# Kernel tuning notes

Hardware: AMD Instinct MI355X
Metric: run time of the kernel (lower is better)

The kernel has to match this reference:

```python
import jax, jax.numpy as jnp
import numpy as np

A_DIM = 6
VBR = jnp.array([300.0, 750.0, 1200.0, 1850.0, 2850.0, 4300.0])
MAX_BR = 4300.0
BUF = 30000.0  # buffer_size fixed to 30000 each forward
N_STEPS = 6    # unrolled iterations in the source (cooked_bw[0]..cooked_bw[5])


def _conv_feat(x, w, b):
    # 1-channel valid Conv1d(kernel=4) + ReLU, flattened channel-major like torch .view
    L = x.shape[0]
    idx = jnp.arange(L - 3)[:, None] + jnp.arange(4)[None, :]
    win = x[idx]                                   # (L-3, 4)
    out = jax.nn.relu(win @ w[:, 0, :].T + b)      # (L-3, 128)
    return out.T.reshape(-1)                       # (128*(L-3),)


def setup_inputs() -> dict:
    key = jax.random.key(0)
    ks = jax.random.split(key, 12)
    s = 0.1
    return {
        "inp": jax.random.uniform(ks[0], (8, 8), jnp.float32) + 0.1,
        "conv_w": jax.random.normal(ks[1], (128, 1, 4), jnp.float32) * s,
        "conv_b": jax.random.normal(ks[2], (128,), jnp.float32) * s,
        "w0": jax.random.normal(ks[3], (128, 1), jnp.float32) * s,
        "b0": jax.random.normal(ks[4], (128,), jnp.float32) * s,
        "w1": jax.random.normal(ks[5], (128, 1), jnp.float32) * s,
        "b1": jax.random.normal(ks[6], (128,), jnp.float32) * s,
        "w2": jax.random.normal(ks[7], (128, 1), jnp.float32) * s,
        "b2": jax.random.normal(ks[8], (128,), jnp.float32) * s,
        "w3": jax.random.normal(ks[9], (128, 2048), jnp.float32) * 0.02,
        "b3": jax.random.normal(ks[10], (128,), jnp.float32) * s,
        "w4": jax.random.normal(ks[11], (6, 128), jnp.float32) * s,
        "b4": jnp.zeros((6,), jnp.float32),
    }


def reference(inp, conv_w, conv_b, w0, b0, w1, b1, w2, b2, w3, b3, w4, b4):
    state = inp[:6, :]          # (6, 8)
    bw = inp[6, :]              # cooked bandwidth trace
    vs = inp[7, 0]              # base video chunk size
    vcs = vs * jnp.array([1.0, 2.0, 4.0, 8.0, 16.0, 32.0])  # video_chunk_sizes

    def net(st):
        s0 = jax.nn.relu(st[0, -1] * w0[:, 0] + b0)
        s1 = jax.nn.relu(st[1, -1] * w1[:, 0] + b1)
        s2 = _conv_feat(st[2, :], conv_w, conv_b)          # 640
        s3 = _conv_feat(st[3, :], conv_w, conv_b)          # 640
        s4 = _conv_feat(st[4, :A_DIM], conv_w, conv_b)     # 384
        s5 = st[4, -1] * w2[:, 0] + b2                     # no relu (matches source)
        feat = jnp.concatenate([s0, s1, s2, s3, s4, s5])   # (2048,)
        h = jax.nn.relu(w3 @ feat + b3)
        return w4 @ h + b4                                 # (6,)

    for i in range(N_STEPS):
        logits = net(state)
        a = jnp.argmax(logits)
        state = jnp.roll(state, -1, axis=1)
        delay = vcs[a] / bw[i] - BUF
        state = state.at[0, -1].set(VBR[a] / MAX_BR)
        state = state.at[1, -1].set(BUF / 1000.0 / 10.0)
        state = state.at[2, -1].set(vcs[a] / delay / 1000.0)
        state = state.at[3, -1].set(delay / 1000.0 / 10.0)
        state = state.at[4, :A_DIM].set(vcs / 1e6)
        state = state.at[5, -1].set((7.0 - i) / 8.0)

    return net(state)
```

## Files before the change

### kernel.cpp

```cpp
#include <hip/hip_runtime.h>

#define NBLK 32
#define TPB  256
#define FSTRIDE 32
#define PSTRIDE 64

__device__ __forceinline__ float relu_(float x) { return fmaxf(x, 0.f); }


__launch_bounds__(TPB, 1)
__global__ void actor_kernel(
    const float* __restrict__ inp,
    const float* __restrict__ conv_w, const float* __restrict__ conv_b,
    const float* __restrict__ w0, const float* __restrict__ b0,
    const float* __restrict__ w1, const float* __restrict__ b1,
    const float* __restrict__ w2, const float* __restrict__ b2,
    const float* __restrict__ w3, const float* __restrict__ b3,
    const float* __restrict__ w4, const float* __restrict__ b4,
    float* __restrict__ out, int* __restrict__ flags,
    float* __restrict__ partials)
{
    const int tid = threadIdx.x;
    const int b   = blockIdx.x;

    __shared__ __align__(16) float lw3[4 * 2048];
    __shared__ __align__(16) float lfeat[2048];
    __shared__ __align__(16) float lc2[512], lc3[512];
    __shared__ float lbase2[128], lbase3[128], ls5[128];
    __shared__ float ls0[6 * 128];
    __shared__ float ltmp[512];
    __shared__ __align__(16) float lcw[512];
    __shared__ float lcb[128];
    __shared__ float lw0v[128], lb0v[128], lw1v[128], lb1v[128];
    __shared__ float lw2v[128], lb2v[128], lb3v[128];
    __shared__ float lw4[768], lb4v[8];
    __shared__ float st2[8], st3[8], st4[8];
    __shared__ float sx[8];
    __shared__ float lbw[8];
    __shared__ float h_lds[4], hv_lds[4 * 8];
    __shared__ float red[48];
    __shared__ float s_red[192];
    __shared__ int   sact[2];

    {
        const float4* g4 = (const float4*)(w3 + b * 4 * 2048);
        float4* l4 = (float4*)lw3;
        for (int idx = tid; idx < 2048; idx += TPB) l4[idx] = g4[idx];
    }
    for (int idx = tid; idx < 512; idx += TPB) lcw[idx] = conv_w[idx];
    if (tid < 128) {
        lcb[tid]  = conv_b[tid];
        lw0v[tid] = w0[tid]; lb0v[tid] = b0[tid];
        lw1v[tid] = w1[tid]; lb1v[tid] = b1[tid];
        lw2v[tid] = w2[tid]; lb2v[tid] = b2[tid];
        lb3v[tid] = b3[tid];
    }
    for (int idx = tid; idx < 768; idx += TPB) lw4[idx] = w4[idx];
    if (tid < 6) lb4v[tid] = b4[tid];
    if (tid < 8) {
        st2[tid] = inp[16 + tid];
        st3[tid] = inp[24 + tid];
        st4[tid] = inp[32 + tid];
        lbw[tid] = inp[48 + tid];
    }
    if (tid == 0) {
        sx[0] = inp[7];   sx[1] = inp[15];
        sx[2] = inp[39];  sx[3] = inp[32];
        sx[4] = inp[56];
    }
    __syncthreads();

    if (tid < 128) {
        const float vb[6] = {300.f, 750.f, 1200.f, 1850.f, 2850.f, 4300.f};
        #pragma unroll
        for (int v = 0; v < 6; ++v)
            ls0[v * 128 + tid] = relu_(vb[v] * (1.f / 4300.f) * lw0v[tid] + lb0v[tid]);
        ltmp[tid] = relu_(3.0f * lw1v[tid] + lb1v[tid]);
    }
    for (int m = tid; m < 384; m += TPB) {
        int c = m / 3, w = m - c * 3;
        float a = lcb[c];
        #pragma unroll
        for (int k = 0; k < 4; ++k)
            a += sx[4] * (float)(1 << (w + k)) * 1e-6f * lcw[c * 4 + k];
        ltmp[128 + m] = relu_(a);
    }
    __syncthreads();

    const int wv = tid >> 6, lane = tid & 63;
    const float* wr = lw3 + wv * 2048;
    const float bias3 = lb3v[b * 4 + wv];

    float hs0p[6], hs14p;
    #pragma unroll
    for (int v = 0; v < 6; ++v)
        hs0p[v] = wr[lane] * ls0[v * 128 + lane] + wr[64 + lane] * ls0[v * 128 + 64 + lane];
    hs14p = wr[128 + lane] * ltmp[lane] + wr[192 + lane] * ltmp[64 + lane];
    #pragma unroll
    for (int k = 0; k < 6; ++k) {
        int m = lane + 64 * k;
        hs14p += wr[1536 + m] * ltmp[128 + m];
    }

    const float VBRc[6] = {300.f, 750.f, 1200.f, 1850.f, 2850.f, 4300.f};

    float fcom_f = 0.f;
    float lb2s[2], lb3s[2], b4f2[2], b4f3[2];
    float cw2s[2], cw3s[2], w32s[2], w33s[2], w42s[2], w43s[2];

    for (int g = 0; g < 3; ++g) {
        const int i = 2 * g;

        if (tid < 128) {
            lfeat[tid]        = relu_(sx[0] * lw0v[tid] + lb0v[tid]);
            lfeat[1920 + tid] =        sx[2] * lw2v[tid] + lb2v[tid];
            lbase2[tid] = st2[5] * lcw[tid*4] + st2[6] * lcw[tid*4+1]
                        + st2[7] * lcw[tid*4+2] + lcb[tid];
            lbase3[tid] = st3[5] * lcw[tid*4] + st3[6] * lcw[tid*4+1]
                        + st3[7] * lcw[tid*4+2] + lcb[tid];
            ls5[tid] = sx[3] * lw2v[tid] + lb2v[tid];
        } else {
            int j = tid - 128;
            lfeat[128 + j] = relu_(sx[1] * lw1v[j] + lb1v[j]);
        }
        for (int m = tid; m < 640; m += TPB) {
            int c = m / 5, w = m - c * 5;
            float a2 = lcb[c], a3 = lcb[c];
            #pragma unroll
            for (int k = 0; k < 4; ++k) {
                float cw = lcw[c * 4 + k];
                a2 += st2[w + k] * cw;
                a3 += st3[w + k] * cw;
            }
            lfeat[256 + m] = relu_(a2);
            lfeat[896 + m] = relu_(a3);
        }
        for (int m = tid; m < 384; m += TPB) {
            int c = m / 3, w = m - c * 3;
            float a4 = lcb[c];
            #pragma unroll
            for (int k = 0; k < 4; ++k) a4 += st4[w + k] * lcw[c * 4 + k];
            lfeat[1536 + m] = relu_(a4);
        }
        for (int m = tid; m < 512; m += TPB) {
            int c = m >> 2, w = m & 3;
            float a2 = lcb[c], a3 = lcb[c];
            #pragma unroll
            for (int k = 0; k < 4; ++k) {
                float cw = lcw[c * 4 + k];
                a2 += st2[w + 1 + k] * cw;
                a3 += st3[w + 1 + k] * cw;
            }
            lc2[m] = relu_(a2);
            lc3[m] = relu_(a3);
        }
        __syncthreads();

        float acc_i;
        {
            const float4* w4p = (const float4*)wr;
            const float4* f4p = (const float4*)lfeat;
            float4 acc = make_float4(0.f, 0.f, 0.f, 0.f);
            #pragma unroll
            for (int it = 0; it < 8; ++it) {
                float4 a = w4p[it * 64 + lane];
                float4 f = f4p[it * 64 + lane];
                acc.x += a.x * f.x; acc.y += a.y * f.y;
                acc.z += a.z * f.z; acc.w += a.w * f.w;
            }
            acc_i = (acc.x + acc.y) + (acc.z + acc.w);
        }

        float s5c = wr[1920 + lane] * ls5[lane] + wr[1984 + lane] * ls5[64 + lane];
        float acc_c = hs14p + s5c;
        #pragma unroll
        for (int k = 0; k < 8; ++k) {
            int m = lane + 64 * k;
            int col = 256 + (m >> 2) * 5 + (m & 3);
            acc_c += wr[col] * lc2[m] + wr[640 + col] * lc3[m];
        }

        float n2[6], n3[6];
        {
            float bwi = lbw[i], vs = sx[4];
            #pragma unroll
            for (int v = 0; v < 6; ++v) {
                float vca   = vs * (float)(1 << v);
                float delay = vca / bwi - 30000.f;
                n2[v] = vca / delay * 1e-3f;
                n3[v] = delay * 1e-4f;
            }
        }
        float accv[6];
        #pragma unroll
        for (int v = 0; v < 6; ++v) accv[v] = hs0p[v];
        #pragma unroll
        for (int t = 0; t < 2; ++t) {
            int c = lane + 64 * t;
            float cw3 = lcw[c * 4 + 3];
            float bb2 = lbase2[c], bb3 = lbase3[c];
            float wc2 = wr[256 + c * 5 + 4], wc3 = wr[896 + c * 5 + 4];
            #pragma unroll
            for (int v = 0; v < 6; ++v)
                accv[v] += relu_(bb2 + n2[v] * cw3) * wc2
                         + relu_(bb3 + n3[v] * cw3) * wc3;
        }

        if (g == 2) {
            fcom_f = hs14p + s5c;
            #pragma unroll
            for (int t = 0; t < 2; ++t) {
                int c = lane + 64 * t;
                float c0 = lcw[c*4], c1 = lcw[c*4+1], c2 = lcw[c*4+2], c3 = lcw[c*4+3];
                cw2s[t] = c2; cw3s[t] = c3;
                lb2s[t] = lbase2[c];  lb3s[t] = lbase3[c];
                b4f2[t] = st2[6]*c0 + st2[7]*c1 + lcb[c];
                b4f3[t] = st3[6]*c0 + st3[7]*c1 + lcb[c];
                w32s[t] = wr[256 + c*5 + 3]; w33s[t] = wr[896 + c*5 + 3];
                w42s[t] = wr[256 + c*5 + 4]; w43s[t] = wr[896 + c*5 + 4];
                #pragma unroll
                for (int w = 0; w < 3; ++w) {
                    float a2 = st2[2+w]*c0 + st2[3+w]*c1 + st2[4+w]*c2 + st2[5+w]*c3 + lcb[c];
                    float a3 = st3[2+w]*c0 + st3[3+w]*c1 + st3[4+w]*c2 + st3[5+w]*c3 + lcb[c];
                    fcom_f += relu_(a2) * wr[256 + c*5 + w] + relu_(a3) * wr[896 + c*5 + w];
                }
            }
        }

        #pragma unroll
        for (int off = 32; off > 0; off >>= 1) {
            acc_i += __shfl_xor(acc_i, off);
            acc_c += __shfl_xor(acc_c, off);
            #pragma unroll
            for (int v = 0; v < 6; ++v) accv[v] += __shfl_xor(accv[v], off);
        }
        if (lane == 0) {
            h_lds[wv] = relu_(acc_i + bias3);
            #pragma unroll
            for (int v = 0; v < 6; ++v)
                hv_lds[wv * 8 + v] = relu_(acc_c + accv[v] + bias3);
        }
        __syncthreads();

        if (tid < 42) {
            int q = tid / 6, t = tid - q * 6;
            float p = 0.f;
            if (q == 0) {
                #pragma unroll
                for (int w = 0; w < 4; ++w) p += lw4[t * 128 + b * 4 + w] * h_lds[w];
            } else {
                #pragma unroll
                for (int w = 0; w < 4; ++w) p += lw4[t * 128 + b * 4 + w] * hv_lds[w * 8 + (q - 1)];
            }
            __hip_atomic_store(&partials[(g * NBLK + b) * PSTRIDE + tid], p,
                               __ATOMIC_RELAXED, __HIP_MEMORY_SCOPE_AGENT);
        }
        __syncthreads();
        if (tid == 0)
            __hip_atomic_store(&flags[b * FSTRIDE], g + 1,
                               __ATOMIC_RELEASE, __HIP_MEMORY_SCOPE_AGENT);
        if (tid < NBLK) {
            while (__hip_atomic_load(&flags[tid * FSTRIDE], __ATOMIC_ACQUIRE,
                                     __HIP_MEMORY_SCOPE_AGENT) < g + 1)
                __builtin_amdgcn_s_sleep(1);
        }
        __syncthreads();

        if (tid < 42) {
            float p = lb4v[tid % 6];
            #pragma unroll
            for (int bb = 0; bb < NBLK; ++bb)
                p += __hip_atomic_load(&partials[(g * NBLK + bb) * PSTRIDE + tid],
                                       __ATOMIC_RELAXED, __HIP_MEMORY_SCOPE_AGENT);
            red[tid] = p;
        }
        __syncthreads();
        if (tid == 0) {
            float best = red[0]; int a0 = 0;
            #pragma unroll
            for (int r = 1; r < 6; ++r) if (red[r] > best) { best = red[r]; a0 = r; }
            best = red[6 + 6 * a0]; int a1 = 0;
            #pragma unroll
            for (int r = 1; r < 6; ++r)
                if (red[6 + 6 * a0 + r] > best) { best = red[6 + 6 * a0 + r]; a1 = r; }

            if (g == 2) {
                sact[0] = a0; sact[1] = a1;
            } else {
                {
                    float vca = sx[4] * (float)(1 << a0);
                    float delay = vca / lbw[i] - 30000.f;
                    sx[0] = VBRc[a0] * (1.f / 4300.f);
                    sx[1] = 3.0f;
                    #pragma unroll
                    for (int c = 0; c < 7; ++c) { st2[c] = st2[c + 1]; st3[c] = st3[c + 1]; }
                    st2[7] = vca / delay * 1e-3f;
                    st3[7] = delay * 1e-4f;
                    sx[2] = sx[3]; sx[3] = sx[4] * 1e-6f;
                    #pragma unroll
                    for (int j = 0; j < 6; ++j) st4[j] = sx[4] * (float)(1 << j) * 1e-6f;
                }
                {
                    float vca = sx[4] * (float)(1 << a1);
                    float delay = vca / lbw[i + 1] - 30000.f;
                    sx[0] = VBRc[a1] * (1.f / 4300.f);
                    sx[1] = 3.0f;
                    #pragma unroll
                    for (int c = 0; c < 7; ++c) { st2[c] = st2[c + 1]; st3[c] = st3[c + 1]; }
                    st2[7] = vca / delay * 1e-3f;
                    st3[7] = delay * 1e-4f;
                    sx[2] = sx[3]; sx[3] = sx[4] * 1e-6f;
                    #pragma unroll
                    for (int j = 0; j < 6; ++j) st4[j] = sx[4] * (float)(1 << j) * 1e-6f;
                }
            }
        }
        __syncthreads();
    }

    {
        const int a4 = sact[0], a5 = sact[1];
        float vs = sx[4];
        float vca4 = vs * (float)(1 << a4);
        float d4   = vca4 / lbw[4] - 30000.f;
        float ap24 = vca4 / d4 * 1e-3f, ap34 = d4 * 1e-4f;
        float vca5 = vs * (float)(1 << a5);
        float d5   = vca5 / lbw[5] - 30000.f;
        float ap25 = vca5 / d5 * 1e-3f, ap35 = d5 * 1e-4f;

        float h0 = hs0p[0];
        h0 = (a5 == 1) ? hs0p[1] : h0;
        h0 = (a5 == 2) ? hs0p[2] : h0;
        h0 = (a5 == 3) ? hs0p[3] : h0;
        h0 = (a5 == 4) ? hs0p[4] : h0;
        h0 = (a5 == 5) ? hs0p[5] : h0;

        float hl = fcom_f + h0;
        #pragma unroll
        for (int t = 0; t < 2; ++t) {
            float r32 = relu_(lb2s[t] + ap24 * cw3s[t]);
            float r33 = relu_(lb3s[t] + ap34 * cw3s[t]);
            float r42 = relu_(b4f2[t] + ap24 * cw2s[t] + ap25 * cw3s[t]);
            float r43 = relu_(b4f3[t] + ap34 * cw2s[t] + ap35 * cw3s[t]);
            hl += r32 * w32s[t] + r33 * w33s[t] + r42 * w42s[t] + r43 * w43s[t];
        }
        #pragma unroll
        for (int off = 32; off > 0; off >>= 1) hl += __shfl_xor(hl, off);
        if (lane == 0) h_lds[wv] = relu_(hl + bias3);
    }
    __syncthreads();
    if (tid < 6) {
        float p = 0.f;
        #pragma unroll
        for (int w = 0; w < 4; ++w) p += lw4[tid * 128 + b * 4 + w] * h_lds[w];
        __hip_atomic_store(&partials[(3 * NBLK + b) * PSTRIDE + tid], p,
                           __ATOMIC_RELAXED, __HIP_MEMORY_SCOPE_AGENT);
    }
    __syncthreads();
    if (tid == 0)
        __hip_atomic_store(&flags[b * FSTRIDE], 4,
                           __ATOMIC_RELEASE, __HIP_MEMORY_SCOPE_AGENT);
    if (b == 0) {
        if (tid < NBLK) {
            while (__hip_atomic_load(&flags[tid * FSTRIDE], __ATOMIC_ACQUIRE,
                                     __HIP_MEMORY_SCOPE_AGENT) < 4)
                __builtin_amdgcn_s_sleep(1);
        }
        __syncthreads();
        if (tid < 192) {
            int j = tid >> 5, bb = tid & 31;
            s_red[j * 32 + bb] =
                __hip_atomic_load(&partials[(3 * NBLK + bb) * PSTRIDE + j],
                                  __ATOMIC_RELAXED, __HIP_MEMORY_SCOPE_AGENT);
        }
        __syncthreads();
        if (tid < 6) {
            float p = lb4v[tid];
            #pragma unroll
            for (int bb = 0; bb < NBLK; ++bb) p += s_red[tid * 32 + bb];
            out[tid] = p;
        }
    }
}

extern "C" void kernel_launch(void* const* d_in, const int* in_sizes, int n_in,
                              void* d_out, int out_size, void* d_ws, size_t ws_size,
                              hipStream_t stream) {
    const float* inp    = (const float*)d_in[0];
    const float* conv_w = (const float*)d_in[1];
    const float* conv_b = (const float*)d_in[2];
    const float* w0     = (const float*)d_in[3];
    const float* b0     = (const float*)d_in[4];
    const float* w1     = (const float*)d_in[5];
    const float* b1     = (const float*)d_in[6];
    const float* w2     = (const float*)d_in[7];
    const float* b2     = (const float*)d_in[8];
    const float* w3     = (const float*)d_in[9];
    const float* b3     = (const float*)d_in[10];
    const float* w4     = (const float*)d_in[11];
    const float* b4     = (const float*)d_in[12];

    int*   flags    = (int*)d_ws;
    float* partials = (float*)((char*)d_ws + 8192);

    actor_kernel<<<NBLK, TPB, 0, stream>>>(inp, conv_w, conv_b,
                                           w0, b0, w1, b1, w2, b2,
                                           w3, b3, w4, b4,
                                           (float*)d_out, flags, partials);
}
```

Before: 99.69 us.

## Speculate final step over all 36 action pairs to drop a grid barrier

In the last group, each block now evaluates the final network output speculatively for all 36 combinations of the last two actions, alongside the existing speculative step. It publishes all partials in one round. Block 0 then resolves both argmaxes and selects the matching final logits. This removes one full cross-block flag barrier and its dependent reduction round. The cost is extra register pressure from 36 accumulators, 36 wave shuffles per offset, and a larger partials buffer and reduction.

```diff
diff --git a/kernel.cpp b/kernel.cpp
--- a/kernel.cpp
+++ b/kernel.cpp
@@ -3,7 +3,7 @@
 #define NBLK 32
 #define TPB  256
 #define FSTRIDE 32
-#define PSTRIDE 64
+#define PSTRIDE 320
 
 __device__ __forceinline__ float relu_(float x) { return fmaxf(x, 0.f); }
 
@@ -38,8 +38,9 @@
     __shared__ float sx[8];
     __shared__ float lbw[8];
     __shared__ float h_lds[4], hv_lds[4 * 8];
+    __shared__ float hfin_lds[4 * 36];
     __shared__ float red[48];
-    __shared__ float s_red[192];
+    __shared__ float s_red[320];
     __shared__ int   sact[2];
 
     {
@@ -103,10 +104,6 @@
     }
 
     const float VBRc[6] = {300.f, 750.f, 1200.f, 1850.f, 2850.f, 4300.f};
-
-    float fcom_f = 0.f;
-    float lb2s[2], lb3s[2], b4f2[2], b4f3[2];
-    float cw2s[2], cw3s[2], w32s[2], w33s[2], w42s[2], w43s[2];
 
     for (int g = 0; g < 3; ++g) {
         const int i = 2 * g;
@@ -207,7 +204,20 @@
         }
 
         if (g == 2) {
-            fcom_f = hs14p + s5c;
+            float ap5[6], ap35[6];
+            {
+                float bw5 = lbw[5], vs = sx[4];
+                #pragma unroll
+                for (int v = 0; v < 6; ++v) {
+                    float vca = vs * (float)(1 << v);
+                    float d   = vca / bw5 - 30000.f;
+                    ap5[v]  = vca / d * 1e-3f;
+                    ap35[v] = d * 1e-4f;
+                }
+            }
+            float fcom = hs14p + s5c;
+            float lb2s[2], lb3s[2], b4f2[2], b4f3[2];
+            float cw2s[2], cw3s[2], w32s[2], w33s[2], w42s[2], w43s[2];
             #pragma unroll
             for (int t = 0; t < 2; ++t) {
                 int c = lane + 64 * t;
@@ -222,8 +232,41 @@
                 for (int w = 0; w < 3; ++w) {
                     float a2 = st2[2+w]*c0 + st2[3+w]*c1 + st2[4+w]*c2 + st2[5+w]*c3 + lcb[c];
                     float a3 = st3[2+w]*c0 + st3[3+w]*c1 + st3[4+w]*c2 + st3[5+w]*c3 + lcb[c];
-                    fcom_f += relu_(a2) * wr[256 + c*5 + w] + relu_(a3) * wr[896 + c*5 + w];
-                }
+                    fcom += relu_(a2) * wr[256 + c*5 + w] + relu_(a3) * wr[896 + c*5 + w];
+                }
+            }
+            float tw3[6];
+            #pragma unroll
+            for (int u = 0; u < 6; ++u) {
+                float s = 0.f;
+                #pragma unroll
+                for (int t = 0; t < 2; ++t)
+                    s += relu_(lb2s[t] + n2[u] * cw3s[t]) * w32s[t]
+                       + relu_(lb3s[t] + n3[u] * cw3s[t]) * w33s[t];
+                tw3[u] = s;
+            }
+            float h36[36];
+            #pragma unroll
+            for (int u = 0; u < 6; ++u) {
+                #pragma unroll
+                for (int v = 0; v < 6; ++v) {
+                    float a = fcom + hs0p[v] + tw3[u];
+                    #pragma unroll
+                    for (int t = 0; t < 2; ++t)
+                        a += relu_(b4f2[t] + n2[u]*cw2s[t] + ap5[v]*cw3s[t]) * w42s[t]
+                           + relu_(b4f3[t] + n3[u]*cw2s[t] + ap35[v]*cw3s[t]) * w43s[t];
+                    h36[u * 6 + v] = a;
+                }
+            }
+            #pragma unroll
+            for (int off = 32; off > 0; off >>= 1) {
+                #pragma unroll
+                for (int m = 0; m < 36; ++m) h36[m] += __shfl_xor(h36[m], off);
+            }
+            if (lane == 0) {
+                #pragma unroll
+                for (int m = 0; m < 36; ++m)
+                    hfin_lds[wv * 36 + m] = relu_(h36[m] + bias3);
             }
         }
 
@@ -242,51 +285,49 @@
         }
         __syncthreads();
 
-        if (tid < 42) {
-            int q = tid / 6, t = tid - q * 6;
-            float p = 0.f;
-            if (q == 0) {
-                #pragma unroll
-                for (int w = 0; w < 4; ++w) p += lw4[t * 128 + b * 4 + w] * h_lds[w];
-            } else {
-                #pragma unroll
-                for (int w = 0; w < 4; ++w) p += lw4[t * 128 + b * 4 + w] * hv_lds[w * 8 + (q - 1)];
-            }
-            __hip_atomic_store(&partials[(g * NBLK + b) * PSTRIDE + tid], p,
-                               __ATOMIC_RELAXED, __HIP_MEMORY_SCOPE_AGENT);
-        }
-        __syncthreads();
-        if (tid == 0)
-            __hip_atomic_store(&flags[b * FSTRIDE], g + 1,
-                               __ATOMIC_RELEASE, __HIP_MEMORY_SCOPE_AGENT);
-        if (tid < NBLK) {
-            while (__hip_atomic_load(&flags[tid * FSTRIDE], __ATOMIC_ACQUIRE,
-                                     __HIP_MEMORY_SCOPE_AGENT) < g + 1)
-                __builtin_amdgcn_s_sleep(1);
-        }
-        __syncthreads();
-
-        if (tid < 42) {
-            float p = lb4v[tid % 6];
-            #pragma unroll
-            for (int bb = 0; bb < NBLK; ++bb)
-                p += __hip_atomic_load(&partials[(g * NBLK + bb) * PSTRIDE + tid],
-                                       __ATOMIC_RELAXED, __HIP_MEMORY_SCOPE_AGENT);
-            red[tid] = p;
-        }
-        __syncthreads();
-        if (tid == 0) {
-            float best = red[0]; int a0 = 0;
-            #pragma unroll
-            for (int r = 1; r < 6; ++r) if (red[r] > best) { best = red[r]; a0 = r; }
-            best = red[6 + 6 * a0]; int a1 = 0;
-            #pragma unroll
-            for (int r = 1; r < 6; ++r)
-                if (red[6 + 6 * a0 + r] > best) { best = red[6 + 6 * a0 + r]; a1 = r; }
-
-            if (g == 2) {
-                sact[0] = a0; sact[1] = a1;
-            } else {
+        if (g < 2) {
+            if (tid < 42) {
+                int q = tid / 6, t = tid - q * 6;
+                float p = 0.f;
+                if (q == 0) {
+                    #pragma unroll
+                    for (int w = 0; w < 4; ++w) p += lw4[t * 128 + b * 4 + w] * h_lds[w];
+                } else {
+                    #pragma unroll
+                    for (int w = 0; w < 4; ++w) p += lw4[t * 128 + b * 4 + w] * hv_lds[w * 8 + (q - 1)];
+                }
+                __hip_atomic_store(&partials[(g * NBLK + b) * PSTRIDE + tid], p,
+                                   __ATOMIC_RELAXED, __HIP_MEMORY_SCOPE_AGENT);
+            }
+            __syncthreads();
+            if (tid == 0)
+                __hip_atomic_store(&flags[b * FSTRIDE], g + 1,
+                                   __ATOMIC_RELEASE, __HIP_MEMORY_SCOPE_AGENT);
+            if (tid < NBLK) {
+                while (__hip_atomic_load(&flags[tid * FSTRIDE], __ATOMIC_ACQUIRE,
+                                         __HIP_MEMORY_SCOPE_AGENT) < g + 1)
+                    __builtin_amdgcn_s_sleep(1);
+            }
+            __syncthreads();
+
+            if (tid < 42) {
+                float p = lb4v[tid % 6];
+                #pragma unroll
+                for (int bb = 0; bb < NBLK; ++bb)
+                    p += __hip_atomic_load(&partials[(g * NBLK + bb) * PSTRIDE + tid],
+                                           __ATOMIC_RELAXED, __HIP_MEMORY_SCOPE_AGENT);
+                red[tid] = p;
+            }
+            __syncthreads();
+            if (tid == 0) {
+                float best = red[0]; int a0 = 0;
+                #pragma unroll
+                for (int r = 1; r < 6; ++r) if (red[r] > best) { best = red[r]; a0 = r; }
+                best = red[6 + 6 * a0]; int a1 = 0;
+                #pragma unroll
+                for (int r = 1; r < 6; ++r)
+                    if (red[6 + 6 * a0 + r] > best) { best = red[6 + 6 * a0 + r]; a1 = r; }
+
                 {
                     float vca = sx[4] * (float)(1 << a0);
                     float delay = vca / lbw[i] - 30000.f;
@@ -314,71 +355,68 @@
                     for (int j = 0; j < 6; ++j) st4[j] = sx[4] * (float)(1 << j) * 1e-6f;
                 }
             }
-        }
-        __syncthreads();
-    }
-
-    {
-        const int a4 = sact[0], a5 = sact[1];
-        float vs = sx[4];
-        float vca4 = vs * (float)(1 << a4);
-        float d4   = vca4 / lbw[4] - 30000.f;
-        float ap24 = vca4 / d4 * 1e-3f, ap34 = d4 * 1e-4f;
-        float vca5 = vs * (float)(1 << a5);
-        float d5   = vca5 / lbw[5] - 30000.f;
-        float ap25 = vca5 / d5 * 1e-3f, ap35 = d5 * 1e-4f;
-
-        float h0 = hs0p[0];
-        h0 = (a5 == 1) ? hs0p[1] : h0;
-        h0 = (a5 == 2) ? hs0p[2] : h0;
-        h0 = (a5 == 3) ? hs0p[3] : h0;
-        h0 = (a5 == 4) ? hs0p[4] : h0;
-        h0 = (a5 == 5) ? hs0p[5] : h0;
-
-        float hl = fcom_f + h0;
-        #pragma unroll
-        for (int t = 0; t < 2; ++t) {
-            float r32 = relu_(lb2s[t] + ap24 * cw3s[t]);
-            float r33 = relu_(lb3s[t] + ap34 * cw3s[t]);
-            float r42 = relu_(b4f2[t] + ap24 * cw2s[t] + ap25 * cw3s[t]);
-            float r43 = relu_(b4f3[t] + ap34 * cw2s[t] + ap35 * cw3s[t]);
-            hl += r32 * w32s[t] + r33 * w33s[t] + r42 * w42s[t] + r43 * w43s[t];
-        }
-        #pragma unroll
-        for (int off = 32; off > 0; off >>= 1) hl += __shfl_xor(hl, off);
-        if (lane == 0) h_lds[wv] = relu_(hl + bias3);
-    }
-    __syncthreads();
-    if (tid < 6) {
-        float p = 0.f;
-        #pragma unroll
-        for (int w = 0; w < 4; ++w) p += lw4[tid * 128 + b * 4 + w] * h_lds[w];
-        __hip_atomic_store(&partials[(3 * NBLK + b) * PSTRIDE + tid], p,
-                           __ATOMIC_RELAXED, __HIP_MEMORY_SCOPE_AGENT);
-    }
-    __syncthreads();
-    if (tid == 0)
-        __hip_atomic_store(&flags[b * FSTRIDE], 4,
-                           __ATOMIC_RELEASE, __HIP_MEMORY_SCOPE_AGENT);
-    if (b == 0) {
-        if (tid < NBLK) {
-            while (__hip_atomic_load(&flags[tid * FSTRIDE], __ATOMIC_ACQUIRE,
-                                     __HIP_MEMORY_SCOPE_AGENT) < 4)
-                __builtin_amdgcn_s_sleep(1);
-        }
-        __syncthreads();
-        if (tid < 192) {
-            int j = tid >> 5, bb = tid & 31;
-            s_red[j * 32 + bb] =
-                __hip_atomic_load(&partials[(3 * NBLK + bb) * PSTRIDE + j],
-                                  __ATOMIC_RELAXED, __HIP_MEMORY_SCOPE_AGENT);
-        }
-        __syncthreads();
-        if (tid < 6) {
-            float p = lb4v[tid];
-            #pragma unroll
-            for (int bb = 0; bb < NBLK; ++bb) p += s_red[tid * 32 + bb];
-            out[tid] = p;
+            __syncthreads();
+        } else {
+            for (int m = tid; m < 258; m += TPB) {
+                float p = 0.f;
+                if (m < 42) {
+                    int q = m / 6, t = m - q * 6;
+                    if (q == 0) {
+                        #pragma unroll
+                        for (int w = 0; w < 4; ++w) p += lw4[t * 128 + b * 4 + w] * h_lds[w];
+                    } else {
+                        #pragma unroll
+                        for (int w = 0; w < 4; ++w) p += lw4[t * 128 + b * 4 + w] * hv_lds[w * 8 + (q - 1)];
+                    }
+                } else {
+                    int c = (m - 42) / 6, t = (m - 42) - c * 6;
+                    #pragma unroll
+                    for (int w = 0; w < 4; ++w) p += lw4[t * 128 + b * 4 + w] * hfin_lds[w * 36 + c];
+                }
+                __hip_atomic_store(&partials[(2 * NBLK + b) * PSTRIDE + m], p,
+                                   __ATOMIC_RELAXED, __HIP_MEMORY_SCOPE_AGENT);
+            }
+            __syncthreads();
+            if (tid == 0)
+                __hip_atomic_store(&flags[b * FSTRIDE], 3,
+                                   __ATOMIC_RELEASE, __HIP_MEMORY_SCOPE_AGENT);
+
+            if (b == 0) {
+                if (tid < NBLK) {
+                    while (__hip_atomic_load(&flags[tid * FSTRIDE], __ATOMIC_ACQUIRE,
+                                             __HIP_MEMORY_SCOPE_AGENT) < 3)
+                        __builtin_amdgcn_s_sleep(1);
+                }
+                __syncthreads();
+                for (int m = tid; m < 258; m += TPB) {
+                    float p = 0.f;
+                    #pragma unroll
+                    for (int bb = 0; bb < NBLK; ++bb)
+                        p += __hip_atomic_load(&partials[(2 * NBLK + bb) * PSTRIDE + m],
+                                               __ATOMIC_RELAXED, __HIP_MEMORY_SCOPE_AGENT);
+                    s_red[m] = p;
+                }
+                __syncthreads();
+                if (tid == 0) {
+                    float best = s_red[0] + lb4v[0]; int a4 = 0;
+                    #pragma unroll
+                    for (int r = 1; r < 6; ++r) {
+                        float v = s_red[r] + lb4v[r];
+                        if (v > best) { best = v; a4 = r; }
+                    }
+                    float best2 = s_red[6 + 6 * a4] + lb4v[0]; int a5 = 0;
+                    #pragma unroll
+                    for (int r = 1; r < 6; ++r) {
+                        float v = s_red[6 + 6 * a4 + r] + lb4v[r];
+                        if (v > best2) { best2 = v; a5 = r; }
+                    }
+                    sact[0] = a4; sact[1] = a5;
+                }
+                __syncthreads();
+                if (tid < 6)
+                    out[tid] = lb4v[tid] +
+                               s_red[42 + (sact[0] * 6 + sact[1]) * 6 + tid];
+            }
         }
     }
 }
```

Result: slower. 106.8 us (+7.1%).

## Collapse inter-block sync and argmax into a single wavefront, prefetch w3 via registers

Applied to the files above, without the earlier changes.

The per-step partial store, flag signal, spin-wait, partial reduction and argmax now run inside wavefront 0 using shuffles instead of LDS plus several block-wide barriers. The final cross-block reduction likewise uses wave shuffles. The w3 slice is loaded into registers early and written to LDS after the small setup work, so global latency overlaps that setup. This removes several __syncthreads on the serial critical path. The cost is more register pressure and reliance on explicit waitcnt ordering for memory visibility.

```diff
diff --git a/kernel.cpp b/kernel.cpp
--- a/kernel.cpp
+++ b/kernel.cpp
@@ -38,15 +38,15 @@
     __shared__ float sx[8];
     __shared__ float lbw[8];
     __shared__ float h_lds[4], hv_lds[4 * 8];
-    __shared__ float red[48];
-    __shared__ float s_red[192];
     __shared__ int   sact[2];
 
+    float4 wreg[8];
     {
         const float4* g4 = (const float4*)(w3 + b * 4 * 2048);
-        float4* l4 = (float4*)lw3;
-        for (int idx = tid; idx < 2048; idx += TPB) l4[idx] = g4[idx];
-    }
+        #pragma unroll
+        for (int it = 0; it < 8; ++it) wreg[it] = g4[it * TPB + tid];
+    }
+
     for (int idx = tid; idx < 512; idx += TPB) lcw[idx] = conv_w[idx];
     if (tid < 128) {
         lcb[tid]  = conv_b[tid];
@@ -84,6 +84,12 @@
         for (int k = 0; k < 4; ++k)
             a += sx[4] * (float)(1 << (w + k)) * 1e-6f * lcw[c * 4 + k];
         ltmp[128 + m] = relu_(a);
+    }
+
+    {
+        float4* l4 = (float4*)lw3;
+        #pragma unroll
+        for (int it = 0; it < 8; ++it) l4[it * TPB + tid] = wreg[it];
     }
     __syncthreads();
 
@@ -242,76 +248,80 @@
         }
         __syncthreads();
 
-        if (tid < 42) {
-            int q = tid / 6, t = tid - q * 6;
+        if (wv == 0) {
+            if (lane < 42) {
+                int q = lane / 6, t = lane - q * 6;
+                float pp = 0.f;
+                if (q == 0) {
+                    #pragma unroll
+                    for (int w = 0; w < 4; ++w) pp += lw4[t * 128 + b * 4 + w] * h_lds[w];
+                } else {
+                    #pragma unroll
+                    for (int w = 0; w < 4; ++w) pp += lw4[t * 128 + b * 4 + w] * hv_lds[w * 8 + (q - 1)];
+                }
+                __hip_atomic_store(&partials[(g * NBLK + b) * PSTRIDE + lane], pp,
+                                   __ATOMIC_RELAXED, __HIP_MEMORY_SCOPE_AGENT);
+            }
+            asm volatile("s_waitcnt vmcnt(0) lgkmcnt(0)" ::: "memory");
+            if (lane == 0)
+                __hip_atomic_store(&flags[b * FSTRIDE], g + 1,
+                                   __ATOMIC_RELEASE, __HIP_MEMORY_SCOPE_AGENT);
+            if (lane < NBLK) {
+                while (__hip_atomic_load(&flags[lane * FSTRIDE], __ATOMIC_ACQUIRE,
+                                         __HIP_MEMORY_SCOPE_AGENT) < g + 1)
+                    __builtin_amdgcn_s_sleep(1);
+            }
             float p = 0.f;
-            if (q == 0) {
+            if (lane < 42) {
+                p = lb4v[lane - (lane / 6) * 6];
                 #pragma unroll
-                for (int w = 0; w < 4; ++w) p += lw4[t * 128 + b * 4 + w] * h_lds[w];
-            } else {
-                #pragma unroll
-                for (int w = 0; w < 4; ++w) p += lw4[t * 128 + b * 4 + w] * hv_lds[w * 8 + (q - 1)];
-            }
-            __hip_atomic_store(&partials[(g * NBLK + b) * PSTRIDE + tid], p,
-                               __ATOMIC_RELAXED, __HIP_MEMORY_SCOPE_AGENT);
-        }
-        __syncthreads();
-        if (tid == 0)
-            __hip_atomic_store(&flags[b * FSTRIDE], g + 1,
-                               __ATOMIC_RELEASE, __HIP_MEMORY_SCOPE_AGENT);
-        if (tid < NBLK) {
-            while (__hip_atomic_load(&flags[tid * FSTRIDE], __ATOMIC_ACQUIRE,
-                                     __HIP_MEMORY_SCOPE_AGENT) < g + 1)
-                __builtin_amdgcn_s_sleep(1);
-        }
-        __syncthreads();
-
-        if (tid < 42) {
-            float p = lb4v[tid % 6];
-            #pragma unroll
-            for (int bb = 0; bb < NBLK; ++bb)
-                p += __hip_atomic_load(&partials[(g * NBLK + bb) * PSTRIDE + tid],
-                                       __ATOMIC_RELAXED, __HIP_MEMORY_SCOPE_AGENT);
-            red[tid] = p;
-        }
-        __syncthreads();
-        if (tid == 0) {
-            float best = red[0]; int a0 = 0;
-            #pragma unroll
-            for (int r = 1; r < 6; ++r) if (red[r] > best) { best = red[r]; a0 = r; }
-            best = red[6 + 6 * a0]; int a1 = 0;
-            #pragma unroll
-            for (int r = 1; r < 6; ++r)
-                if (red[6 + 6 * a0 + r] > best) { best = red[6 + 6 * a0 + r]; a1 = r; }
-
-            if (g == 2) {
-                sact[0] = a0; sact[1] = a1;
-            } else {
-                {
-                    float vca = sx[4] * (float)(1 << a0);
-                    float delay = vca / lbw[i] - 30000.f;
-                    sx[0] = VBRc[a0] * (1.f / 4300.f);
-                    sx[1] = 3.0f;
-                    #pragma unroll
-                    for (int c = 0; c < 7; ++c) { st2[c] = st2[c + 1]; st3[c] = st3[c + 1]; }
-                    st2[7] = vca / delay * 1e-3f;
-                    st3[7] = delay * 1e-4f;
-                    sx[2] = sx[3]; sx[3] = sx[4] * 1e-6f;
-                    #pragma unroll
-                    for (int j = 0; j < 6; ++j) st4[j] = sx[4] * (float)(1 << j) * 1e-6f;
-                }
-                {
-                    float vca = sx[4] * (float)(1 << a1);
-                    float delay = vca / lbw[i + 1] - 30000.f;
-                    sx[0] = VBRc[a1] * (1.f / 4300.f);
-                    sx[1] = 3.0f;
-                    #pragma unroll
-                    for (int c = 0; c < 7; ++c) { st2[c] = st2[c + 1]; st3[c] = st3[c + 1]; }
-                    st2[7] = vca / delay * 1e-3f;
-                    st3[7] = delay * 1e-4f;
-                    sx[2] = sx[3]; sx[3] = sx[4] * 1e-6f;
-                    #pragma unroll
-                    for (int j = 0; j < 6; ++j) st4[j] = sx[4] * (float)(1 << j) * 1e-6f;
+                for (int bb = 0; bb < NBLK; ++bb)
+                    p += __hip_atomic_load(&partials[(g * NBLK + bb) * PSTRIDE + lane],
+                                           __ATOMIC_RELAXED, __HIP_MEMORY_SCOPE_AGENT);
+            }
+            float q0[6];
+            #pragma unroll
+            for (int r = 0; r < 6; ++r) q0[r] = __shfl(p, r);
+            int a0 = 0; float best = q0[0];
+            #pragma unroll
+            for (int r = 1; r < 6; ++r) if (q0[r] > best) { best = q0[r]; a0 = r; }
+            float q1[6];
+            #pragma unroll
+            for (int r = 0; r < 6; ++r) q1[r] = __shfl(p, 6 + 6 * a0 + r);
+            int a1 = 0; best = q1[0];
+            #pragma unroll
+            for (int r = 1; r < 6; ++r) if (q1[r] > best) { best = q1[r]; a1 = r; }
+
+            if (lane == 0) {
+                if (g == 2) {
+                    sact[0] = a0; sact[1] = a1;
+                } else {
+                    {
+                        float vca = sx[4] * (float)(1 << a0);
+                        float delay = vca / lbw[i] - 30000.f;
+                        sx[0] = VBRc[a0] * (1.f / 4300.f);
+                        sx[1] = 3.0f;
+                        #pragma unroll
+                        for (int c = 0; c < 7; ++c) { st2[c] = st2[c + 1]; st3[c] = st3[c + 1]; }
+                        st2[7] = vca / delay * 1e-3f;
+                        st3[7] = delay * 1e-4f;
+                        sx[2] = sx[3]; sx[3] = sx[4] * 1e-6f;
+                        #pragma unroll
+                        for (int j = 0; j < 6; ++j) st4[j] = sx[4] * (float)(1 << j) * 1e-6f;
+                    }
+                    {
+                        float vca = sx[4] * (float)(1 << a1);
+                        float delay = vca / lbw[i + 1] - 30000.f;
+                        sx[0] = VBRc[a1] * (1.f / 4300.f);
+                        sx[1] = 3.0f;
+                        #pragma unroll
+                        for (int c = 0; c < 7; ++c) { st2[c] = st2[c + 1]; st3[c] = st3[c + 1]; }
+                        st2[7] = vca / delay * 1e-3f;
+                        st3[7] = delay * 1e-4f;
+                        sx[2] = sx[3]; sx[3] = sx[4] * 1e-6f;
+                        #pragma unroll
+                        for (int j = 0; j < 6; ++j) st4[j] = sx[4] * (float)(1 << j) * 1e-6f;
+                    }
                 }
             }
         }
@@ -349,36 +359,42 @@
         if (lane == 0) h_lds[wv] = relu_(hl + bias3);
     }
     __syncthreads();
-    if (tid < 6) {
-        float p = 0.f;
-        #pragma unroll
-        for (int w = 0; w < 4; ++w) p += lw4[tid * 128 + b * 4 + w] * h_lds[w];
-        __hip_atomic_store(&partials[(3 * NBLK + b) * PSTRIDE + tid], p,
-                           __ATOMIC_RELAXED, __HIP_MEMORY_SCOPE_AGENT);
-    }
-    __syncthreads();
-    if (tid == 0)
-        __hip_atomic_store(&flags[b * FSTRIDE], 4,
-                           __ATOMIC_RELEASE, __HIP_MEMORY_SCOPE_AGENT);
-    if (b == 0) {
-        if (tid < NBLK) {
-            while (__hip_atomic_load(&flags[tid * FSTRIDE], __ATOMIC_ACQUIRE,
-                                     __HIP_MEMORY_SCOPE_AGENT) < 4)
-                __builtin_amdgcn_s_sleep(1);
-        }
-        __syncthreads();
-        if (tid < 192) {
-            int j = tid >> 5, bb = tid & 31;
-            s_red[j * 32 + bb] =
-                __hip_atomic_load(&partials[(3 * NBLK + bb) * PSTRIDE + j],
-                                  __ATOMIC_RELAXED, __HIP_MEMORY_SCOPE_AGENT);
-        }
-        __syncthreads();
-        if (tid < 6) {
-            float p = lb4v[tid];
-            #pragma unroll
-            for (int bb = 0; bb < NBLK; ++bb) p += s_red[tid * 32 + bb];
-            out[tid] = p;
+
+    if (wv == 0) {
+        if (lane < 6) {
+            float pv = 0.f;
+            #pragma unroll
+            for (int w = 0; w < 4; ++w) pv += lw4[lane * 128 + b * 4 + w] * h_lds[w];
+            __hip_atomic_store(&partials[(3 * NBLK + b) * PSTRIDE + lane], pv,
+                               __ATOMIC_RELAXED, __HIP_MEMORY_SCOPE_AGENT);
+        }
+        asm volatile("s_waitcnt vmcnt(0) lgkmcnt(0)" ::: "memory");
+        if (lane == 0)
+            __hip_atomic_store(&flags[b * FSTRIDE], 4,
+                               __ATOMIC_RELEASE, __HIP_MEMORY_SCOPE_AGENT);
+        if (b == 0) {
+            if (lane < NBLK) {
+                while (__hip_atomic_load(&flags[lane * FSTRIDE], __ATOMIC_ACQUIRE,
+                                         __HIP_MEMORY_SCOPE_AGENT) < 4)
+                    __builtin_amdgcn_s_sleep(1);
+            }
+            float s[6] = {0.f, 0.f, 0.f, 0.f, 0.f, 0.f};
+            if (lane < NBLK) {
+                const float* src = &partials[(3 * NBLK + lane) * PSTRIDE];
+                #pragma unroll
+                for (int j = 0; j < 6; ++j)
+                    s[j] = __hip_atomic_load(&src[j], __ATOMIC_RELAXED,
+                                             __HIP_MEMORY_SCOPE_AGENT);
+            }
+            #pragma unroll
+            for (int off = 16; off > 0; off >>= 1) {
+                #pragma unroll
+                for (int j = 0; j < 6; ++j) s[j] += __shfl_xor(s[j], off);
+            }
+            if (lane == 0) {
+                #pragma unroll
+                for (int j = 0; j < 6; ++j) out[j] = lb4v[j] + s[j];
+            }
         }
     }
 }
```

Measured after the change: 101.5 us. No clear change (+1.8%).
